# Kernel optimization log

Measured on AMD Instinct MI355X. Metric: run time of the kernel, lower is better.

Reference implementation:

```python
import jax, jax.numpy as jnp
import numpy as np

D = 256          # common_dim = specific_dim
NH = 8           # num_heads
HD = D // NH     # head_dim = 32
B, S = 16, 1024
EPS = 1e-5


def _mha(q, k, v, wq, bq, wk, bk, wv, bv, wo, bo):
    # q,k,v: [B, S, D]; weights stored [in, out] so y = x @ w + b
    b_, _, _ = q.shape

    def proj(x, w, b):
        return (x @ w + b).reshape(b_, -1, NH, HD).transpose(0, 2, 1, 3)  # [B,H,S,hd]

    Q, K, V = proj(q, wq, bq), proj(k, wk, bk), proj(v, wv, bv)
    scores = jnp.einsum('bhqd,bhkd->bhqk', Q, K) / (float(HD) ** 0.5)
    attn = jax.nn.softmax(scores, axis=-1)
    out = jnp.einsum('bhqk,bhkd->bhqd', attn, V)
    out = out.transpose(0, 2, 1, 3).reshape(b_, -1, D)
    return out @ wo + bo


def _ln(x, g, b):
    mu = jnp.mean(x, axis=-1, keepdims=True)
    var = jnp.var(x, axis=-1, keepdims=True)
    return (x - mu) * jax.lax.rsqrt(var + EPS) * g + b


def setup_inputs() -> dict:
    key = jax.random.key(0)
    ks = iter(jax.random.split(key, 32))
    rn = lambda *shape: jax.random.normal(next(ks), shape, dtype=jnp.float32)
    w = lambda i, o: rn(i, o) * 0.05
    inp = {
        'img_common': rn(B, S, D),
        'txt_common': rn(B, S, D),
        'img_specific': rn(B, D),
        'txt_specific': rn(B, D),
    }
    for pfx in ('i2t', 't2i'):
        for nm in ('q', 'k', 'v', 'o'):
            inp[f'{pfx}_w{nm}'] = w(D, D)
            inp[f'{pfx}_b{nm}'] = jnp.zeros((D,), jnp.float32)
    inp['ln_img_g'] = jnp.ones((D,), jnp.float32)
    inp['ln_img_b'] = jnp.zeros((D,), jnp.float32)
    inp['ln_txt_g'] = jnp.ones((D,), jnp.float32)
    inp['ln_txt_b'] = jnp.zeros((D,), jnp.float32)
    inp['enh_w'] = w(2 * D, D)
    inp['enh_b'] = jnp.zeros((D,), jnp.float32)
    inp['inc_w'] = w(2 * D, D)
    inp['inc_b'] = jnp.zeros((D,), jnp.float32)
    return inp


def reference(img_common, txt_common, img_specific, txt_specific,
              i2t_wq, i2t_bq, i2t_wk, i2t_bk, i2t_wv, i2t_bv, i2t_wo, i2t_bo,
              t2i_wq, t2i_bq, t2i_wk, t2i_bk, t2i_wv, t2i_bv, t2i_wo, t2i_bo,
              ln_img_g, ln_img_b, ln_txt_g, ln_txt_b,
              enh_w, enh_b, inc_w, inc_b):
    att_i2t = _mha(img_common, txt_common, txt_common,
                   i2t_wq, i2t_bq, i2t_wk, i2t_bk, i2t_wv, i2t_bv, i2t_wo, i2t_bo)
    img_query = _ln(att_i2t + img_common, ln_img_g, ln_img_b)
    att_t2i = _mha(txt_common, img_common, img_common,
                   t2i_wq, t2i_bq, t2i_wk, t2i_bk, t2i_wv, t2i_bv, t2i_wo, t2i_bo)
    txt_query = _ln(att_t2i + txt_common, ln_txt_g, ln_txt_b)
    combined = jnp.concatenate((img_query, txt_query), axis=-1)  # [B,S,2D]
    enhancement = combined @ enh_w + enh_b                        # [B,S,D]
    inc = jnp.concatenate((img_specific - txt_specific,
                           img_specific * txt_specific), axis=1)  # [B,2D]
    inconsistency = inc @ inc_w + inc_b                           # [B,D]
    return (enhancement, inconsistency, img_specific, txt_specific)
```

## Files before the change

### kernel.cpp

```cpp
#include <hip/hip_runtime.h>
#include <stdint.h>

typedef unsigned int u32;
typedef unsigned short u16;
typedef __attribute__((ext_vector_type(8))) short bf16x8;
typedef __attribute__((ext_vector_type(4))) float f32x4;

#define BUF_ELEMS (16384 * 256)

__device__ __forceinline__ float bflo(u32 u) { return __uint_as_float(u << 16); }
__device__ __forceinline__ float bfhi(u32 u) { return __uint_as_float(u & 0xffff0000u); }
__device__ __forceinline__ u16 f2bf(float f) {
    u32 u = __float_as_uint(f);
    return (u16)((u + 0x7fffu + ((u >> 16) & 1u)) >> 16);
}
__device__ __forceinline__ u32 pkhi(float lo, float hi) {
    return __builtin_amdgcn_perm(__float_as_uint(hi), __float_as_uint(lo), 0x07060302u);
}
__device__ __forceinline__ float fexp2(float x) {
#if __has_builtin(__builtin_amdgcn_exp2f)
    return __builtin_amdgcn_exp2f(x);
#else
    float r; asm("v_exp_f32 %0, %1" : "=v"(r) : "v"(x)); return r;
#endif
}
__device__ __forceinline__ float frcp(float x) {
#if __has_builtin(__builtin_amdgcn_rcpf)
    return __builtin_amdgcn_rcpf(x);
#else
    return 1.f / x;
#endif
}

struct WT {
    const float* src[9];
    u16* dst[9];
    const float* bs[6];
    float* bA;
    float* bB;
    const float* img_sp;
    const float* txt_sp;
    const float* incw;
    const float* incb;
    float* out_inc;
    float* out_img;
    float* out_txt;
};

__global__ __launch_bounds__(256)
void wtrans_kernel(WT wt)
{
    __shared__ float T[64][65];
    const int bid = blockIdx.x, t = threadIdx.x;
    if (bid == 160) {
        wt.bA[t]       = wt.bs[0][t];
        wt.bA[256 + t] = wt.bs[1][t];
        wt.bA[512 + t] = wt.bs[2][t];
        wt.bB[t]       = wt.bs[3][t];
        wt.bB[256 + t] = wt.bs[4][t];
        wt.bB[512 + t] = wt.bs[5][t];
        return;
    }
    if (bid > 160) {
        float* iv = &T[0][0];
        const int b = bid - 161, n = t;
        float a = wt.img_sp[b * 256 + n];
        float x = wt.txt_sp[b * 256 + n];
        iv[n] = a - x;
        iv[256 + n] = a * x;
        __syncthreads();
        float acc = wt.incb[n];
        for (int k = 0; k < 512; k++) acc += iv[k] * wt.incw[k * 256 + n];
        wt.out_inc[b * 256 + n] = acc;
        wt.out_img[b * 256 + n] = a;
        wt.out_txt[b * 256 + n] = x;
        return;
    }
    int m, sub;
    if (bid < 128) { m = bid >> 4; sub = bid & 15; }
    else           { m = 8;        sub = bid - 128; }
    const int K = (m == 8) ? 512 : 256;
    const int kt = (m == 8) ? (sub & 7) : (sub & 3);
    const int nt = (m == 8) ? (sub >> 3) : (sub >> 2);
    const int k0 = kt * 64, n0 = nt * 64;
    const float* src = wt.src[m];
    u16* dst = wt.dst[m];

    const int kk = t >> 2, nn = (t & 3) * 16;
    #pragma unroll
    for (int j = 0; j < 16; j += 4) {
        float4 v = *(const float4*)(src + (size_t)(k0 + kk) * 256 + n0 + nn + j);
        T[kk][nn + j + 0] = v.x; T[kk][nn + j + 1] = v.y;
        T[kk][nn + j + 2] = v.z; T[kk][nn + j + 3] = v.w;
    }
    __syncthreads();
    const int nn2 = t >> 2, kc = (t & 3) * 16;
    #pragma unroll
    for (int j = 0; j < 16; j++)
        dst[(size_t)(n0 + nn2) * K + k0 + kc + j] = f2bf(T[kc + j][nn2]);
}

template<int MODE>
__global__ __launch_bounds__(256)
void gemm_mfma(const float* __restrict__ Af0, const float* __restrict__ Af1,
               const u16* __restrict__ Ab0, const u16* __restrict__ Ab1,
               const u16* __restrict__ Wt0, const u16* __restrict__ Wt1,
               const float* __restrict__ bias0, const float* __restrict__ bias1,
               void* __restrict__ o0, void* __restrict__ o1, void* __restrict__ o2,
               void* __restrict__ o3, void* __restrict__ o4, void* __restrict__ o5)
{
    __shared__ u16 As[128][72];
    __shared__ u16 Bs[128][72];
    const int tid = threadIdx.x;
    const int wave = tid >> 6, lane = tid & 63;
    const int L = lane & 15, Qd = lane >> 4;
    int m_idx, n_idx;
    if (MODE == 0)      { m_idx = blockIdx.x & 255; n_idx = blockIdx.x >> 8; }
    else if (MODE == 1) { m_idx = blockIdx.x & 255; n_idx = blockIdx.x >> 8; }
    else                { m_idx = blockIdx.x & 127; n_idx = blockIdx.x >> 7; }
    const bool ms = (MODE == 0 || MODE == 1) ? (m_idx >= 128) : false;
    const int lm0 = (MODE == 2) ? m_idx * 128 : (m_idx & 127) * 128;
    const int n0 = n_idx * 128;
    const u16* Wt = ms ? Wt1 : Wt0;
    const float* bias = ms ? bias1 : bias0;
    const int wr = wave & 1, wc = wave >> 1;
    const int sr = tid >> 1, sh = (tid & 1) * 32;
    const int KS = (MODE == 2) ? 512 : 256;

    f32x4 acc[4][4] = {};

    for (int kt = 0; kt < KS; kt += 64) {
        if (MODE == 0) {
            const float* Af = ms ? Af1 : Af0;
            const float* Ap = Af + (size_t)(lm0 + sr) * 256 + kt + sh;
            uint4 pk[2];
            #pragma unroll
            for (int half = 0; half < 2; half++) {
                float4 f0 = *(const float4*)(Ap + half * 16);
                float4 f1 = *(const float4*)(Ap + half * 16 + 4);
                float4 f2 = *(const float4*)(Ap + half * 16 + 8);
                float4 f3 = *(const float4*)(Ap + half * 16 + 12);
                pk[half].x = pkhi(f0.x, f0.y);
                pk[half].y = pkhi(f0.z, f0.w);
                pk[half].z = pkhi(f1.x, f1.y);
                pk[half].w = pkhi(f1.z, f1.w);
                uint4 q;
                q.x = pkhi(f2.x, f2.y); q.y = pkhi(f2.z, f2.w);
                q.z = pkhi(f3.x, f3.y); q.w = pkhi(f3.z, f3.w);
                *(uint4*)&As[sr][sh + half * 16 + 8] = q;
            }
            *(uint4*)&As[sr][sh + 0] = pk[0];
            *(uint4*)&As[sr][sh + 16] = pk[1];
        } else {
            const u16* Abase;
            int lkt = kt;
            if (MODE == 2) { Abase = (kt < 256) ? Ab0 : Ab1; lkt = kt & 255; }
            else           { Abase = ms ? Ab1 : Ab0; }
            const u16* Ap = Abase + (size_t)(lm0 + sr) * 256 + lkt + sh;
            uint4 a0 = *(const uint4*)(Ap + 0);
            uint4 a1 = *(const uint4*)(Ap + 8);
            uint4 a2 = *(const uint4*)(Ap + 16);
            uint4 a3 = *(const uint4*)(Ap + 24);
            *(uint4*)&As[sr][sh + 0]  = a0;
            *(uint4*)&As[sr][sh + 8]  = a1;
            *(uint4*)&As[sr][sh + 16] = a2;
            *(uint4*)&As[sr][sh + 24] = a3;
        }
        {
            const u16* Bp = Wt + (size_t)(n0 + sr) * KS + kt + sh;
            uint4 w0 = *(const uint4*)(Bp + 0);
            uint4 w1 = *(const uint4*)(Bp + 8);
            uint4 w2 = *(const uint4*)(Bp + 16);
            uint4 w3 = *(const uint4*)(Bp + 24);
            *(uint4*)&Bs[sr][sh + 0]  = w0;
            *(uint4*)&Bs[sr][sh + 8]  = w1;
            *(uint4*)&Bs[sr][sh + 16] = w2;
            *(uint4*)&Bs[sr][sh + 24] = w3;
        }
        __syncthreads();
        #pragma unroll
        for (int kh = 0; kh < 64; kh += 32) {
            bf16x8 af[4], bf[4];
            #pragma unroll
            for (int mt = 0; mt < 4; mt++)
                af[mt] = *(const bf16x8*)&As[wr * 64 + mt * 16 + L][kh + Qd * 8];
            #pragma unroll
            for (int nt = 0; nt < 4; nt++)
                bf[nt] = *(const bf16x8*)&Bs[wc * 64 + nt * 16 + L][kh + Qd * 8];
            #pragma unroll
            for (int mt = 0; mt < 4; mt++)
                #pragma unroll
                for (int nt = 0; nt < 4; nt++)
                    acc[mt][nt] = __builtin_amdgcn_mfma_f32_16x16x32_bf16(
                        af[mt], bf[nt], acc[mt][nt], 0, 0, 0);
        }
        __syncthreads();
    }

    float bvals[4];
    #pragma unroll
    for (int nt = 0; nt < 4; nt++)
        bvals[nt] = bias[n0 + wc * 64 + nt * 16 + L];

    const float qsc = (MODE == 0 && n_idx < 2)
                      ? (0.17677669529663687f * 1.4426950408889634f) : 1.0f;

    void* outp;
    int colb;
    if (MODE == 0) {
        const int g = n_idx >> 1;
        if (!ms) outp = (g == 0) ? o0 : ((g == 1) ? o1 : o2);
        else     outp = (g == 0) ? o3 : ((g == 1) ? o4 : o5);
        colb = (n_idx & 1) * 128 + wc * 64;
    } else if (MODE == 1) {
        outp = ms ? o1 : o0;
        colb = n0 + wc * 64;
    } else {
        outp = o0;
        colb = n0 + wc * 64;
    }

    if (MODE == 0 && n_idx >= 4) {
        u16* Vg = (u16*)outp;
        #pragma unroll
        for (int mt = 0; mt < 4; mt++) {
            const int tokb = lm0 + wr * 64 + mt * 16 + Qd * 4;
            const int b_ = tokb >> 10;
            const int s_ = tokb & 1023;
            #pragma unroll
            for (int nt = 0; nt < 4; nt++) {
                const int col = colb + nt * 16 + L;
                const int h_ = col >> 5, d_ = col & 31;
                uint2 pk2;
                pk2.x = (u32)f2bf(acc[mt][nt][0] + bvals[nt])
                      | ((u32)f2bf(acc[mt][nt][1] + bvals[nt]) << 16);
                pk2.y = (u32)f2bf(acc[mt][nt][2] + bvals[nt])
                      | ((u32)f2bf(acc[mt][nt][3] + bvals[nt]) << 16);
                *(uint2*)(Vg + ((size_t)((b_ * 8 + h_) * 32 + d_) << 10) + s_) = pk2;
            }
        }
        return;
    }

    #pragma unroll
    for (int mt = 0; mt < 4; mt++) {
        #pragma unroll
        for (int r = 0; r < 4; r++) {
            const size_t row = (size_t)(lm0 + wr * 64 + mt * 16 + Qd * 4 + r) * 256;
            #pragma unroll
            for (int nt = 0; nt < 4; nt++) {
                const int col = colb + nt * 16 + L;
                float v = (acc[mt][nt][r] + bvals[nt]) * qsc;
                if (MODE == 2) ((float*)outp)[row + col] = v;
                else           ((u16*)outp)[row + col] = f2bf(v);
            }
        }
    }
}

__global__ __launch_bounds__(256, 4)
void attn_mfma(const u16* __restrict__ Q0, const u16* __restrict__ K0,
               const u16* __restrict__ V0, u16* __restrict__ O0,
               const u16* __restrict__ Q1, const u16* __restrict__ K1,
               const u16* __restrict__ V1, u16* __restrict__ O1)
{
    __shared__ u16 Ks[128][40];
    __shared__ u16 Vt[32][136];
    const int tid = threadIdx.x;
    const int wave = tid >> 6, lane = tid & 63;
    const int L = lane & 15, Qd = lane >> 4;
    const int bid = blockIdx.x;
    const int qt = (bid >> 3) & 7;
    const int kv = (bid & 7) | ((bid >> 6) << 3);
    const int set = kv >> 7;
    const int b = (kv >> 3) & 15;
    const int h = kv & 7;
    const u16* Q = set ? Q1 : Q0;
    const u16* K = set ? K1 : K0;
    const u16* V = set ? V1 : V0;
    u16* O = set ? O1 : O0;
    const int rowbase = b * 1024;
    const int qbase = rowbase + qt * 128;

    bf16x8 qfrag[2];
    #pragma unroll
    for (int qs = 0; qs < 2; qs++)
        qfrag[qs] = *(const bf16x8*)(Q + (size_t)(qbase + qs * 64 + wave * 16 + L) * 256
                                       + h * 32 + Qd * 8);

    const short oneb = (short)0x3F80;
    const bf16x8 ones = {oneb, oneb, oneb, oneb, oneb, oneb, oneb, oneb};

    f32x4 oaccT[2][2] = {};
    f32x4 oaccL[2] = {};

    const int s     = tid >> 1;
    const int kkey  = (s & 3) | (((s >> 3) & 1) << 2) | (((s >> 2) & 1) << 3)
                    | (((s >> 4) & 1) << 4) | ((s >> 5) << 5);
    const int kcolh = (tid & 1) * 16;
    const int krow  = (kkey & 96) | (((kkey >> 2) & 1) << 4)
                    | (((kkey >> 3) & 3) << 2) | (kkey & 3);
    const int vd    = tid >> 3;
    const int vkb   = (tid & 7) * 16;
    const size_t vplane = (size_t)((b * 8 + h) * 32 + vd) * 1024;

    uint4 kr0, kr1, vr0, vr1;
    {
        const size_t kb = (size_t)(rowbase + kkey) * 256 + h * 32 + kcolh;
        kr0 = *(const uint4*)(K + kb);
        kr1 = *(const uint4*)(K + kb + 8);
        const size_t vb = vplane + vkb;
        vr0 = *(const uint4*)(V + vb);
        vr1 = *(const uint4*)(V + vb + 8);
    }

    for (int t = 0; t < 8; t++) {
        *(uint4*)&Ks[krow][kcolh]     = kr0;
        *(uint4*)&Ks[krow][kcolh + 8] = kr1;
        *(uint4*)&Vt[vd][vkb]         = vr0;
        *(uint4*)&Vt[vd][vkb + 8]     = vr1;
        __syncthreads();

        if (t < 7) {
            const size_t kb = (size_t)(rowbase + (t + 1) * 128 + kkey) * 256 + h * 32 + kcolh;
            kr0 = *(const uint4*)(K + kb);
            kr1 = *(const uint4*)(K + kb + 8);
            const size_t vb = vplane + (t + 1) * 128 + vkb;
            vr0 = *(const uint4*)(V + vb);
            vr1 = *(const uint4*)(V + vb + 8);
        }

        bf16x8 kf[8];
        #pragma unroll
        for (int ct = 0; ct < 8; ct++)
            kf[ct] = *(const bf16x8*)&Ks[ct * 16 + L][Qd * 8];

        bf16x8 vfr[4][2];
        #pragma unroll
        for (int kc = 0; kc < 4; kc++) {
            vfr[kc][0] = *(const bf16x8*)&Vt[L][kc * 32 + Qd * 8];
            vfr[kc][1] = *(const bf16x8*)&Vt[16 + L][kc * 32 + Qd * 8];
        }

        #pragma unroll
        for (int qs = 0; qs < 2; qs++) {
            const f32x4 z = {0.f, 0.f, 0.f, 0.f};
            #pragma unroll
            for (int kc = 0; kc < 4; kc++) {
                f32x4 s0 = __builtin_amdgcn_mfma_f32_16x16x32_bf16(kf[2 * kc],     qfrag[qs], z, 0, 0, 0);
                f32x4 s1 = __builtin_amdgcn_mfma_f32_16x16x32_bf16(kf[2 * kc + 1], qfrag[qs], z, 0, 0, 0);
                union { u32 w[4]; bf16x8 v; } pf;
                pf.w[0] = pkhi(fexp2(s0[0]), fexp2(s0[1]));
                pf.w[1] = pkhi(fexp2(s0[2]), fexp2(s0[3]));
                pf.w[2] = pkhi(fexp2(s1[0]), fexp2(s1[1]));
                pf.w[3] = pkhi(fexp2(s1[2]), fexp2(s1[3]));
                oaccT[qs][0] = __builtin_amdgcn_mfma_f32_16x16x32_bf16(vfr[kc][0], pf.v, oaccT[qs][0], 0, 0, 0);
                oaccT[qs][1] = __builtin_amdgcn_mfma_f32_16x16x32_bf16(vfr[kc][1], pf.v, oaccT[qs][1], 0, 0, 0);
                oaccL[qs]    = __builtin_amdgcn_mfma_f32_16x16x32_bf16(ones,       pf.v, oaccL[qs],    0, 0, 0);
            }
        }
        __syncthreads();
    }

    #pragma unroll
    for (int qs = 0; qs < 2; qs++) {
        float inv = frcp(oaccL[qs][0]);
        u16* op = O + (size_t)(qbase + qs * 64 + wave * 16 + L) * 256 + h * 32 + Qd * 4;
        #pragma unroll
        for (int db = 0; db < 2; db++) {
            uint2 w;
            w.x = (u32)f2bf(oaccT[qs][db][0] * inv)
                | ((u32)f2bf(oaccT[qs][db][1] * inv) << 16);
            w.y = (u32)f2bf(oaccT[qs][db][2] * inv)
                | ((u32)f2bf(oaccT[qs][db][3] * inv) << 16);
            *(uint2*)(op + db * 16) = w;
        }
    }
}

__global__ __launch_bounds__(256)
void ln_res_kernel(const u16* __restrict__ P0, const u16* __restrict__ P1,
                   const float* __restrict__ R0, const float* __restrict__ R1,
                   const float* __restrict__ g0, const float* __restrict__ be0,
                   const float* __restrict__ g1, const float* __restrict__ be1,
                   u16* __restrict__ out0, u16* __restrict__ out1)
{
    const int lane = threadIdx.x & 63;
    int row = blockIdx.x * 4 + (threadIdx.x >> 6);
    const bool sel = row >= 16384;
    const u16* P = sel ? P1 : P0;
    const float* R = sel ? R1 : R0;
    const float* g = sel ? g1 : g0;
    const float* be = sel ? be1 : be0;
    u16* out = sel ? out1 : out0;
    if (sel) row -= 16384;
    const int col = lane * 4;
    uint2 pv = *(const uint2*)(P + (size_t)row * 256 + col);
    float4 rv = *(const float4*)(R + (size_t)row * 256 + col);
    float x0 = bflo(pv.x) + rv.x;
    float x1 = bfhi(pv.x) + rv.y;
    float x2 = bflo(pv.y) + rv.z;
    float x3 = bfhi(pv.y) + rv.w;
    float s = x0 + x1 + x2 + x3;
    float s2 = x0*x0 + x1*x1 + x2*x2 + x3*x3;
    #pragma unroll
    for (int off = 32; off > 0; off >>= 1) {
        s  += __shfl_xor(s, off);
        s2 += __shfl_xor(s2, off);
    }
    float mean = s * 0.00390625f;
    float var = fmaxf(s2 * 0.00390625f - mean * mean, 0.f);
    float rstd = rsqrtf(var + 1e-5f);
    float4 gv = *(const float4*)(g + col);
    float4 bv = *(const float4*)(be + col);
    uint2 pk;
    pk.x = (u32)f2bf((x0 - mean) * rstd * gv.x + bv.x)
         | ((u32)f2bf((x1 - mean) * rstd * gv.y + bv.y) << 16);
    pk.y = (u32)f2bf((x2 - mean) * rstd * gv.z + bv.z)
         | ((u32)f2bf((x3 - mean) * rstd * gv.w + bv.w) << 16);
    *(uint2*)(out + (size_t)row * 256 + col) = pk;
}

extern "C" void kernel_launch(void* const* d_in, const int* in_sizes, int n_in,
                              void* d_out, int out_size, void* d_ws, size_t ws_size,
                              hipStream_t stream)
{
    (void)in_sizes; (void)n_in; (void)out_size; (void)ws_size;
    const float* img    = (const float*)d_in[0];
    const float* txt    = (const float*)d_in[1];
    const float* img_sp = (const float*)d_in[2];
    const float* txt_sp = (const float*)d_in[3];
    const float* wq_i = (const float*)d_in[4];  const float* bq_i = (const float*)d_in[5];
    const float* wk_i = (const float*)d_in[6];  const float* bk_i = (const float*)d_in[7];
    const float* wv_i = (const float*)d_in[8];  const float* bv_i = (const float*)d_in[9];
    const float* wo_i = (const float*)d_in[10]; const float* bo_i = (const float*)d_in[11];
    const float* wq_t = (const float*)d_in[12]; const float* bq_t = (const float*)d_in[13];
    const float* wk_t = (const float*)d_in[14]; const float* bk_t = (const float*)d_in[15];
    const float* wv_t = (const float*)d_in[16]; const float* bv_t = (const float*)d_in[17];
    const float* wo_t = (const float*)d_in[18]; const float* bo_t = (const float*)d_in[19];
    const float* lng_i = (const float*)d_in[20]; const float* lnb_i = (const float*)d_in[21];
    const float* lng_t = (const float*)d_in[22]; const float* lnb_t = (const float*)d_in[23];
    const float* enh_w = (const float*)d_in[24]; const float* enh_b = (const float*)d_in[25];
    const float* incw  = (const float*)d_in[26]; const float* incb  = (const float*)d_in[27];
    float* out = (float*)d_out;
    u16* wsp = (u16*)d_ws;
    u16* B0 = wsp;
    u16* B1 = wsp + 1 * (size_t)BUF_ELEMS;
    u16* B2 = wsp + 2 * (size_t)BUF_ELEMS;
    u16* B3 = wsp + 3 * (size_t)BUF_ELEMS;
    u16* B4 = wsp + 4 * (size_t)BUF_ELEMS;
    u16* B5 = wsp + 5 * (size_t)BUF_ELEMS;
    u16* wbase = wsp + 6 * (size_t)BUF_ELEMS;
    u16* WtA   = wbase;
    u16* WtB   = wbase + 196608;
    u16* Wt_oi = wbase + 393216;
    u16* Wt_ot = wbase + 458752;
    u16* Wt_en = wbase + 524288;
    float* biasA = (float*)(wbase + 655360);
    float* biasB = biasA + 768;

    dim3 blk(256);
    WT wt;
    wt.src[0] = wq_i; wt.dst[0] = WtA;
    wt.src[1] = wk_t; wt.dst[1] = WtA + 65536;
    wt.src[2] = wv_t; wt.dst[2] = WtA + 131072;
    wt.src[3] = wq_t; wt.dst[3] = WtB;
    wt.src[4] = wk_i; wt.dst[4] = WtB + 65536;
    wt.src[5] = wv_i; wt.dst[5] = WtB + 131072;
    wt.src[6] = wo_i; wt.dst[6] = Wt_oi;
    wt.src[7] = wo_t; wt.dst[7] = Wt_ot;
    wt.src[8] = enh_w; wt.dst[8] = Wt_en;
    wt.bs[0] = bq_i; wt.bs[1] = bk_t; wt.bs[2] = bv_t;
    wt.bs[3] = bq_t; wt.bs[4] = bk_i; wt.bs[5] = bv_i;
    wt.bA = biasA; wt.bB = biasB;
    wt.img_sp = img_sp; wt.txt_sp = txt_sp; wt.incw = incw; wt.incb = incb;
    wt.out_inc = out + 4194304; wt.out_img = out + 4198400; wt.out_txt = out + 4202496;
    wtrans_kernel<<<177, blk, 0, stream>>>(wt);

    gemm_mfma<0><<<1536, blk, 0, stream>>>(img, txt, nullptr, nullptr,
                                           WtA, WtB, biasA, biasB,
                                           B0, B4, B5, B3, B1, B2);
    attn_mfma<<<2048, blk, 0, stream>>>(B0, B1, B2, B0, B3, B4, B5, B3);
    gemm_mfma<1><<<512, blk, 0, stream>>>(nullptr, nullptr, B0, B3,
                                          Wt_oi, Wt_ot, bo_i, bo_t,
                                          B1, B4, nullptr, nullptr, nullptr, nullptr);
    ln_res_kernel<<<8192, blk, 0, stream>>>(B1, B4, img, txt,
                                            lng_i, lnb_i, lng_t, lnb_t, B2, B5);
    gemm_mfma<2><<<256, blk, 0, stream>>>(nullptr, nullptr, B2, B5,
                                          Wt_en, nullptr, enh_b, nullptr,
                                          out, nullptr, nullptr, nullptr, nullptr, nullptr);
}
```

Measured before the change: 264.4 us.

## Prefetch next GEMM K-tile into registers and swizzle block order for weight reuse

The GEMM main loop now issues the global loads for the next 64-wide K tile into registers right after the shared-memory barrier, so they overlap the MFMA work on the current tile. The block index mapping is also changed so that groups of eight consecutive blocks share the same N tile and sweep M together, which is meant to improve L2 reuse of A and W tiles. The cost is extra register pressure from the prefetch buffers, which could reduce occupancy, especially in MODE 0 where 32 fp32 values per thread are held.

```diff
diff --git a/kernel.cpp b/kernel.cpp
--- a/kernel.cpp
+++ b/kernel.cpp
@@ -114,11 +114,12 @@
     const int tid = threadIdx.x;
     const int wave = tid >> 6, lane = tid & 63;
     const int L = lane & 15, Qd = lane >> 4;
-    int m_idx, n_idx;
-    if (MODE == 0)      { m_idx = blockIdx.x & 255; n_idx = blockIdx.x >> 8; }
-    else if (MODE == 1) { m_idx = blockIdx.x & 255; n_idx = blockIdx.x >> 8; }
-    else                { m_idx = blockIdx.x & 127; n_idx = blockIdx.x >> 7; }
-    const bool ms = (MODE == 0 || MODE == 1) ? (m_idx >= 128) : false;
+    const int NC = (MODE == 0) ? 6 : 2;
+    const int x_ = blockIdx.x & 7;
+    const int r_ = blockIdx.x >> 3;
+    const int n_idx = r_ % NC;
+    const int m_idx = x_ + ((r_ / NC) << 3);
+    const bool ms = (MODE != 2) && (m_idx >= 128);
     const int lm0 = (MODE == 2) ? m_idx * 128 : (m_idx & 127) * 128;
     const int n0 = n_idx * 128;
     const u16* Wt = ms ? Wt1 : Wt0;
@@ -129,55 +130,56 @@
 
     f32x4 acc[4][4] = {};
 
+    float4 fr[8];
+    uint4  ar[4];
+    uint4  br[4];
+
+#define GEMM_LOAD(ktv)                                                        \
+    do {                                                                      \
+        if (MODE == 0) {                                                      \
+            const float* Af = ms ? Af1 : Af0;                                 \
+            const float* Ap = Af + (size_t)(lm0 + sr) * 256 + (ktv) + sh;     \
+            _Pragma("unroll")                                                 \
+            for (int i = 0; i < 8; i++) fr[i] = *(const float4*)(Ap + i * 4); \
+        } else {                                                              \
+            const u16* Abase; int lkt = (ktv);                                \
+            if (MODE == 2) { Abase = ((ktv) < 256) ? Ab0 : Ab1; lkt = (ktv) & 255; } \
+            else           { Abase = ms ? Ab1 : Ab0; }                        \
+            const u16* Ap = Abase + (size_t)(lm0 + sr) * 256 + lkt + sh;      \
+            _Pragma("unroll")                                                 \
+            for (int i = 0; i < 4; i++) ar[i] = *(const uint4*)(Ap + i * 8);  \
+        }                                                                     \
+        const u16* Bp = Wt + (size_t)(n0 + sr) * KS + (ktv) + sh;             \
+        _Pragma("unroll")                                                     \
+        for (int i = 0; i < 4; i++) br[i] = *(const uint4*)(Bp + i * 8);      \
+    } while (0)
+
+    GEMM_LOAD(0);
+
     for (int kt = 0; kt < KS; kt += 64) {
         if (MODE == 0) {
-            const float* Af = ms ? Af1 : Af0;
-            const float* Ap = Af + (size_t)(lm0 + sr) * 256 + kt + sh;
-            uint4 pk[2];
             #pragma unroll
             for (int half = 0; half < 2; half++) {
-                float4 f0 = *(const float4*)(Ap + half * 16);
-                float4 f1 = *(const float4*)(Ap + half * 16 + 4);
-                float4 f2 = *(const float4*)(Ap + half * 16 + 8);
-                float4 f3 = *(const float4*)(Ap + half * 16 + 12);
-                pk[half].x = pkhi(f0.x, f0.y);
-                pk[half].y = pkhi(f0.z, f0.w);
-                pk[half].z = pkhi(f1.x, f1.y);
-                pk[half].w = pkhi(f1.z, f1.w);
-                uint4 q;
+                float4 f0 = fr[half * 4 + 0], f1 = fr[half * 4 + 1];
+                float4 f2 = fr[half * 4 + 2], f3 = fr[half * 4 + 3];
+                uint4 p, q;
+                p.x = pkhi(f0.x, f0.y); p.y = pkhi(f0.z, f0.w);
+                p.z = pkhi(f1.x, f1.y); p.w = pkhi(f1.z, f1.w);
                 q.x = pkhi(f2.x, f2.y); q.y = pkhi(f2.z, f2.w);
                 q.z = pkhi(f3.x, f3.y); q.w = pkhi(f3.z, f3.w);
+                *(uint4*)&As[sr][sh + half * 16 + 0] = p;
                 *(uint4*)&As[sr][sh + half * 16 + 8] = q;
             }
-            *(uint4*)&As[sr][sh + 0] = pk[0];
-            *(uint4*)&As[sr][sh + 16] = pk[1];
         } else {
-            const u16* Abase;
-            int lkt = kt;
-            if (MODE == 2) { Abase = (kt < 256) ? Ab0 : Ab1; lkt = kt & 255; }
-            else           { Abase = ms ? Ab1 : Ab0; }
-            const u16* Ap = Abase + (size_t)(lm0 + sr) * 256 + lkt + sh;
-            uint4 a0 = *(const uint4*)(Ap + 0);
-            uint4 a1 = *(const uint4*)(Ap + 8);
-            uint4 a2 = *(const uint4*)(Ap + 16);
-            uint4 a3 = *(const uint4*)(Ap + 24);
-            *(uint4*)&As[sr][sh + 0]  = a0;
-            *(uint4*)&As[sr][sh + 8]  = a1;
-            *(uint4*)&As[sr][sh + 16] = a2;
-            *(uint4*)&As[sr][sh + 24] = a3;
-        }
-        {
-            const u16* Bp = Wt + (size_t)(n0 + sr) * KS + kt + sh;
-            uint4 w0 = *(const uint4*)(Bp + 0);
-            uint4 w1 = *(const uint4*)(Bp + 8);
-            uint4 w2 = *(const uint4*)(Bp + 16);
-            uint4 w3 = *(const uint4*)(Bp + 24);
-            *(uint4*)&Bs[sr][sh + 0]  = w0;
-            *(uint4*)&Bs[sr][sh + 8]  = w1;
-            *(uint4*)&Bs[sr][sh + 16] = w2;
-            *(uint4*)&Bs[sr][sh + 24] = w3;
-        }
+            #pragma unroll
+            for (int i = 0; i < 4; i++) *(uint4*)&As[sr][sh + i * 8] = ar[i];
+        }
+        #pragma unroll
+        for (int i = 0; i < 4; i++) *(uint4*)&Bs[sr][sh + i * 8] = br[i];
         __syncthreads();
+
+        if (kt + 64 < KS) GEMM_LOAD(kt + 64);
+
         #pragma unroll
         for (int kh = 0; kh < 64; kh += 32) {
             bf16x8 af[4], bf[4];
@@ -196,6 +198,7 @@
         }
         __syncthreads();
     }
+#undef GEMM_LOAD
 
     float bvals[4];
     #pragma unroll
```

Measured after the change: 322.6 us. 1.22x slower.
